# Optimization experiments

Hardware: AMD Instinct MI355X
Metric: run time of the kernel (lower is better)

Reference implementation:

```python
import jax, jax.numpy as jnp
import numpy as np

NUM_HEADS = 16
THETA = 1000.0


def apply_rope(x, positions, theta):
    """x: [B, H, S, d_k]; positions: [S] float. Interleaved-pair RoPE."""
    d = x.shape[-1]
    inv_freq = theta ** (-jnp.arange(0, d, 2, dtype=x.dtype) / d)  # [d/2]
    ang = positions[:, None] * inv_freq[None, :]                    # [S, d/2]
    cos, sin = jnp.cos(ang), jnp.sin(ang)
    x1, x2 = x[..., 0::2], x[..., 1::2]
    r1 = x1 * cos - x2 * sin
    r2 = x1 * sin + x2 * cos
    return jnp.stack([r1, r2], axis=-1).reshape(x.shape)


def setup_inputs() -> dict:
    key = jax.random.key(0)
    ks = jax.random.split(key, 5)
    B, S, D = 2, 2048, 1024
    scale = 1.0 / np.sqrt(D)
    return {
        "in_features": jax.random.normal(ks[0], (B, S, D), jnp.float32),
        "q_proj_weight": jax.random.normal(ks[1], (D, D), jnp.float32) * scale,
        "k_proj_weight": jax.random.normal(ks[2], (D, D), jnp.float32) * scale,
        "v_proj_weight": jax.random.normal(ks[3], (D, D), jnp.float32) * scale,
        "o_proj_weight": jax.random.normal(ks[4], (D, D), jnp.float32) * scale,
        "token_positions": jnp.arange(S, dtype=jnp.int32),
    }


def reference(in_features, q_proj_weight, k_proj_weight, v_proj_weight,
              o_proj_weight, token_positions):
    B, S, D = in_features.shape
    H = NUM_HEADS
    d_k = D // H

    # Original rearrange: '(d_k heads) d_model -> heads d_model d_k'
    # => first dim splits as [d_k, heads] (heads is the inner factor).
    def split_heads(w):
        return w.reshape(d_k, H, D).transpose(1, 2, 0)  # [H, D, d_k]

    Wq, Wk, Wv = split_heads(q_proj_weight), split_heads(k_proj_weight), split_heads(v_proj_weight)

    xq = jnp.einsum("bsd,hdk->bhsk", in_features, Wq)
    xk = jnp.einsum("bsd,hdk->bhsk", in_features, Wk)
    xv = jnp.einsum("bsd,hdk->bhsk", in_features, Wv)

    pos = token_positions.astype(in_features.dtype)
    xq = apply_rope(xq, pos, THETA)
    xk = apply_rope(xk, pos, THETA)

    scores = jnp.einsum("bhqk,bhmk->bhqm", xq, xk) / jnp.sqrt(
        jnp.asarray(d_k, in_features.dtype))
    causal_mask = jnp.triu(jnp.ones((S, S), bool), k=1)  # True above diagonal
    scores = jnp.where(causal_mask, -jnp.inf, scores)
    attn = jax.nn.softmax(scores, axis=-1)

    out = jnp.einsum("bhqm,bhmv->bhqv", attn, xv)        # [B, H, S, d_k]
    out = out.transpose(0, 2, 1, 3).reshape(B, S, D)     # (heads d_emb) concat
    return out @ o_proj_weight                            # [B, S, d_o]
```

## Files before the change

### kernel.cpp

```cpp
#include <hip/hip_runtime.h>

typedef unsigned short u16;
typedef unsigned int u32;
typedef __bf16 bf16x8 __attribute__((ext_vector_type(8)));
typedef float f32x4 __attribute__((ext_vector_type(4)));

#define SEQ 2048
#define DMODEL 1024
#define NH 16
#define DK 64
#define BATCH 2
#define MTOT (BATCH * SEQ)

__device__ __forceinline__ u16 f2b(float f) {
  u32 u = __float_as_uint(f);
  u += 0x7fffu + ((u >> 16) & 1u);
  return (u16)(u >> 16);
}

__device__ __forceinline__ u32 cvtpk(float lo, float hi) {
  u32 r;
  asm("v_cvt_pk_bf16_f32 %0, %1, %2" : "=v"(r) : "v"(lo), "v"(hi));
  return r;
}

__device__ __forceinline__ void gload16(const void* g, void* l) {
  __builtin_amdgcn_global_load_lds((const __attribute__((address_space(1))) u32*)g,
                                   (__attribute__((address_space(3))) u32*)l, 16, 0, 0);
}

__global__ __launch_bounds__(256) void cvt_bf16(const float* __restrict__ in,
                                                u16* __restrict__ out, int n4) {
  int i = blockIdx.x * 256 + threadIdx.x;
  if (i < n4) {
    float4 v = ((const float4*)in)[i];
    uint2 o;
    o.x = (u32)f2b(v.x) | ((u32)f2b(v.y) << 16);
    o.y = (u32)f2b(v.z) | ((u32)f2b(v.w) << 16);
    ((uint2*)out)[i] = o;
  }
}

__global__ __launch_bounds__(256) void cvt_w3(const float* __restrict__ wq,
                                              const float* __restrict__ wk,
                                              const float* __restrict__ wv,
                                              u16* __restrict__ oq,
                                              u16* __restrict__ ok,
                                              u16* __restrict__ ov) {
  const int m = blockIdx.y;
  const float* in = (m == 0) ? wq : ((m == 1) ? wk : wv);
  u16* out = (m == 0) ? oq : ((m == 1) ? ok : ov);
  const int i = blockIdx.x * 256 + threadIdx.x;
  float4 v = ((const float4*)in)[i];
  uint2 o;
  o.x = (u32)f2b(v.x) | ((u32)f2b(v.y) << 16);
  o.y = (u32)f2b(v.z) | ((u32)f2b(v.w) << 16);
  ((uint2*)out)[i] = o;
}

__global__ __launch_bounds__(256) void rope_tab_k(const int* __restrict__ tokpos,
                                                  float2* __restrict__ tab) {
  const int i = blockIdx.x * 256 + threadIdx.x;
  const int s = i >> 5, Xi = i & 31;
  const float invf = powf(1000.0f, -(float)Xi / 32.0f);
  const float ang = (float)tokpos[s] * invf;
  float sn, cs;
  sincosf(ang, &sn, &cs);
  tab[i] = make_float2(cs, sn);
}

__global__ __launch_bounds__(256) void transpose_wo(const float* __restrict__ wo,
                                                    u16* __restrict__ wot) {
  __shared__ float tile[32][33];
  const int bx = blockIdx.x * 32;
  const int by = blockIdx.y * 32;
  const int tx = threadIdx.x & 31, ty = threadIdx.x >> 5;
  for (int j = ty; j < 32; j += 8)
    tile[j][tx] = wo[(size_t)(by + j) * DMODEL + bx + tx];
  __syncthreads();
  for (int j = ty; j < 32; j += 8)
    wot[(size_t)(bx + j) * DMODEL + by + tx] = f2b(tile[tx][j]);
}

__device__ __forceinline__ void qkv_core(const u16* __restrict__ A,
                                         const u16* __restrict__ Bt,
                                         int mbase, int nbase,
                                         u16* As, u16* Bs, f32x4 acc[4][4]) {
  const int t = threadIdx.x;
  const int lane = t & 63, w = t >> 6;
  const int wr = w >> 1, wc = w & 1;
  const int l15 = lane & 15, lg = lane >> 4;
  const int srow = t >> 3;
  const int sch = (t & 7) ^ (srow & 7);
  const int rsw = l15 & 7;
  const int ASZ = 128 * 64;
  const int NIT = DMODEL / 64;

  auto stage = [&](int bufsel, int kb) {
    u16* Ad = &As[bufsel * ASZ];
    u16* Bd = &Bs[bufsel * ASZ];
#pragma unroll
    for (int j = 0; j < 4; ++j)
      gload16(&A[(size_t)(mbase + srow + 32 * j) * DMODEL + kb + sch * 8],
              &Ad[j * 2048 + t * 8]);
#pragma unroll
    for (int j = 0; j < 4; ++j)
      gload16(&Bt[(size_t)(nbase + srow + 32 * j) * DMODEL + kb + sch * 8],
              &Bd[j * 2048 + t * 8]);
  };

  auto compute = [&](int bufsel) {
    const u16* Ac = &As[bufsel * ASZ];
    const u16* Bc = &Bs[bufsel * ASZ];
#pragma unroll
    for (int kk = 0; kk < 2; ++kk) {
      bf16x8 af[4], bfr[4];
#pragma unroll
      for (int mi = 0; mi < 4; ++mi) {
        const int row = wr * 64 + mi * 16 + l15;
        af[mi] = *(const bf16x8*)&Ac[row * 64 + (((kk * 4 + lg) ^ rsw) * 8)];
      }
#pragma unroll
      for (int ni = 0; ni < 4; ++ni) {
        const int row = wc * 64 + ni * 16 + l15;
        bfr[ni] = *(const bf16x8*)&Bc[row * 64 + (((kk * 4 + lg) ^ rsw) * 8)];
      }
#pragma unroll
      for (int mi = 0; mi < 4; ++mi)
#pragma unroll
        for (int ni = 0; ni < 4; ++ni)
          acc[mi][ni] =
              __builtin_amdgcn_mfma_f32_16x16x32_bf16(af[mi], bfr[ni], acc[mi][ni], 0, 0, 0);
    }
  };

  stage(0, 0);

  for (int it = 0; it < NIT - 1; ++it) {
    const int buf = it & 1;
    stage(buf ^ 1, (it + 1) * 64);
    __builtin_amdgcn_sched_barrier(0);
    asm volatile("s_waitcnt vmcnt(8)" ::: "memory");
    __builtin_amdgcn_sched_barrier(0);
    __builtin_amdgcn_s_barrier();
    __builtin_amdgcn_sched_barrier(0);
    compute(buf);
    __builtin_amdgcn_sched_barrier(0);
    __builtin_amdgcn_s_barrier();
  }
  asm volatile("s_waitcnt vmcnt(0)" ::: "memory");
  __builtin_amdgcn_sched_barrier(0);
  __builtin_amdgcn_s_barrier();
  __builtin_amdgcn_sched_barrier(0);
  compute((DMODEL / 64 - 1) & 1);
}

__global__ __launch_bounds__(256) void gemm_qkv(
    const u16* __restrict__ Xb, const u16* __restrict__ Wqb,
    const u16* __restrict__ Wkb, const u16* __restrict__ Wvb,
    u16* __restrict__ Qb, u16* __restrict__ Kb, u16* __restrict__ Vb,
    const float2* __restrict__ tab) {
  __shared__ __align__(16) u16 As[2 * 128 * 64];
  __shared__ __align__(16) u16 Bs[2 * 128 * 64];

  const int mat = blockIdx.y >> 3;
  const int nbase = (blockIdx.y & 7) * 128;
  const int mbase = blockIdx.x * 128;
  const u16* Bt = (mat == 0) ? Wqb : ((mat == 1) ? Wkb : Wvb);

  f32x4 acc[4][4];
#pragma unroll
  for (int mi = 0; mi < 4; ++mi)
#pragma unroll
    for (int ni = 0; ni < 4; ++ni) {
      f32x4 z = {0.f, 0.f, 0.f, 0.f};
      acc[mi][ni] = z;
    }

  qkv_core(Xb, Bt, mbase, nbase, As, Bs, acc);

  const int t = threadIdx.x;
  const int lane = t & 63, w = t >> 6;
  const int wr = w >> 1, wc = w & 1;
  const int l15 = lane & 15, lg = lane >> 4;

  if (mat == 2) {
#pragma unroll
    for (int mi = 0; mi < 4; ++mi) {
#pragma unroll
      for (int r = 0; r < 4; ++r) {
        const int row = mbase + wr * 64 + mi * 16 + lg * 4 + r;
        const int bi = row >> 11, s = row & (SEQ - 1);
#pragma unroll
        for (int ni = 0; ni < 4; ++ni) {
          const int c = nbase + wc * 64 + ni * 16 + l15;
          const int hh = c & 15, vd = c >> 4;
          Vb[((size_t)((bi * NH + hh) * DK + vd)) * SEQ + s] = f2b(acc[mi][ni][r]);
        }
      }
    }
  } else {
    u16* Ob = (mat == 0) ? Qb : Kb;
    const float qscale = (mat == 0) ? 0.125f * 1.44269504088896f : 1.0f;
#pragma unroll
    for (int ni = 0; ni < 4; ni += 2) {
      const int Xi = (nbase + wc * 64 + ni * 16) >> 5;
#pragma unroll
      for (int mi = 0; mi < 4; ++mi) {
#pragma unroll
        for (int r = 0; r < 4; ++r) {
          const int row = mbase + wr * 64 + mi * 16 + lg * 4 + r;
          const int bi = row >> 11, s = row & (SEQ - 1);
          const float2 ct = tab[(s << 5) + Xi];
          const float x1 = acc[mi][ni][r], x2 = acc[mi][ni + 1][r];
          const float r1 = (x1 * ct.x - x2 * ct.y) * qscale;
          const float r2 = (x1 * ct.y + x2 * ct.x) * qscale;
          const u32 pk = (u32)f2b(r1) | ((u32)f2b(r2) << 16);
          *(u32*)&Ob[((size_t)((bi * NH + l15) * SEQ + s) << 6) + (Xi << 1)] = pk;
        }
      }
    }
  }
}

__global__ __launch_bounds__(256) void flash_attn(
    const u16* __restrict__ Qg, const u16* __restrict__ Kg,
    const u16* __restrict__ VTg, u16* __restrict__ Ag) {
  __shared__ __align__(16) u16 Ks[2][64 * 64];
  __shared__ __align__(16) u16 Vs[2][80 * 64];
  __shared__ __align__(16) u16 Ps[4][16][72];

  const int id = blockIdx.y * 32 + blockIdx.x;
  const int within = id >> 3;
  const int bh = (id & 7) * 4 + (within & 3);
  const int qt = 31 - (within >> 2);
  const int b = bh >> 4, h = bh & 15;
  const int qbase = qt * 64;

  const size_t hoff = (size_t)bh * SEQ * DK;
  const u16* Qh = Qg + hoff;
  const u16* Kh = Kg + hoff;
  const u16* VTh = VTg + hoff;

  const int t = threadIdx.x;
  const int lane = t & 63, w = t >> 6;
  const int l15 = lane & 15, lg = lane >> 4;
  const int sw = l15 & 7;

  for (int i = t; i < 2 * 16 * 64; i += 256) {
    const int bufi = i >> 10, rr = (i >> 6) & 15, cc = i & 63;
    Vs[bufi][(64 + rr) * 64 + cc] = (rr == 0) ? (u16)0x3F80 : (u16)0;
  }

  const int qrow = qbase + w * 16 + l15;
  const bf16x8 qf0 = *(const bf16x8*)&Qh[(size_t)qrow * DK + lg * 8];
  const bf16x8 qf1 = *(const bf16x8*)&Qh[(size_t)qrow * DK + 32 + lg * 8];

  f32x4 oaccT[4];
  f32x4 oacc5;
#pragma unroll
  for (int vf = 0; vf < 4; ++vf) {
    f32x4 z = {0.f, 0.f, 0.f, 0.f};
    oaccT[vf] = z;
  }
  {
    f32x4 z = {0.f, 0.f, 0.f, 0.f};
    oacc5 = z;
  }

  const int srow = t >> 3;
  const int sc = ((t & 7) ^ (srow & 7)) * 8;

  auto stageKV = [&](int bufsel, int kb) {
    gload16(&Kh[(size_t)(kb + srow) * DK + sc], &Ks[bufsel][t * 8]);
    gload16(&Kh[(size_t)(kb + srow + 32) * DK + sc], &Ks[bufsel][2048 + t * 8]);
    gload16(&VTh[(size_t)srow * SEQ + kb + sc], &Vs[bufsel][t * 8]);
    gload16(&VTh[(size_t)(srow + 32) * SEQ + kb + sc], &Vs[bufsel][2048 + t * 8]);
  };

  stageKV(0, 0);

  for (int kt = 0; kt <= qt; ++kt) {
    const int buf = kt & 1;
    if (kt < qt) {
      stageKV(buf ^ 1, (kt + 1) * 64);
      __builtin_amdgcn_sched_barrier(0);
      asm volatile("s_waitcnt vmcnt(4)" ::: "memory");
    } else {
      __builtin_amdgcn_sched_barrier(0);
      asm volatile("s_waitcnt vmcnt(0)" ::: "memory");
    }
    __builtin_amdgcn_sched_barrier(0);
    __builtin_amdgcn_s_barrier();
    __builtin_amdgcn_sched_barrier(0);

    const int kvbase = kt * 64;

    f32x4 sT[4];
    __builtin_amdgcn_s_setprio(1);
#pragma unroll
    for (int f = 0; f < 4; ++f) {
      const int row = f * 16 + l15;
      bf16x8 k0 = *(const bf16x8*)&Ks[buf][row * 64 + (lg ^ sw) * 8];
      bf16x8 k1 = *(const bf16x8*)&Ks[buf][row * 64 + ((4 + lg) ^ sw) * 8];
      f32x4 z = {0.f, 0.f, 0.f, 0.f};
      z = __builtin_amdgcn_mfma_f32_16x16x32_bf16(k0, qf0, z, 0, 0, 0);
      z = __builtin_amdgcn_mfma_f32_16x16x32_bf16(k1, qf1, z, 0, 0, 0);
      sT[f] = z;
    }
    __builtin_amdgcn_s_setprio(0);

    if (kt == qt) {
#pragma unroll
      for (int f = 0; f < 4; ++f)
#pragma unroll
        for (int r = 0; r < 4; ++r) {
          const int kvc = kvbase + f * 16 + lg * 4 + r;
          if (kvc > qrow) sT[f][r] = -1e30f;
        }
    }

#pragma unroll
    for (int f = 0; f < 4; ++f)
#pragma unroll
      for (int r = 0; r < 4; ++r) sT[f][r] = exp2f(sT[f][r]);

#pragma unroll
    for (int f = 0; f < 4; ++f) {
      uint2 pkv;
      pkv.x = cvtpk(sT[f][0], sT[f][1]);
      pkv.y = cvtpk(sT[f][2], sT[f][3]);
      *(uint2*)&Ps[w][l15][f * 16 + lg * 4] = pkv;
    }

    __builtin_amdgcn_s_setprio(1);
#pragma unroll
    for (int c = 0; c < 2; ++c) {
      const bf16x8 pb = *(const bf16x8*)&Ps[w][l15][c * 32 + lg * 8];
#pragma unroll
      for (int vf = 0; vf < 4; ++vf) {
        const bf16x8 va =
            *(const bf16x8*)&Vs[buf][(vf * 16 + l15) * 64 + ((c * 4 + lg) ^ sw) * 8];
        oaccT[vf] = __builtin_amdgcn_mfma_f32_16x16x32_bf16(va, pb, oaccT[vf], 0, 0, 0);
      }
      const bf16x8 va5 =
          *(const bf16x8*)&Vs[buf][(64 + l15) * 64 + ((c * 4 + lg) ^ sw) * 8];
      oacc5 = __builtin_amdgcn_mfma_f32_16x16x32_bf16(va5, pb, oacc5, 0, 0, 0);
    }
    __builtin_amdgcn_s_setprio(0);

    __builtin_amdgcn_sched_barrier(0);
    __builtin_amdgcn_s_barrier();
  }

  const float l = __shfl(oacc5[0], l15);
  const float inv = 1.0f / l;
  const size_t base = ((size_t)(b * SEQ + qrow)) * DMODEL + h * DK;
#pragma unroll
  for (int vf = 0; vf < 4; ++vf) {
    uint2 ov;
    ov.x = cvtpk(oaccT[vf][0] * inv, oaccT[vf][1] * inv);
    ov.y = cvtpk(oaccT[vf][2] * inv, oaccT[vf][3] * inv);
    *(uint2*)&Ag[base + vf * 16 + lg * 4] = ov;
  }
}

__global__ __launch_bounds__(256) void gemm_out(const u16* __restrict__ Ab,
                                                const u16* __restrict__ Wotb,
                                                float* __restrict__ Co) {
  __shared__ __align__(16) u16 As[64 * 64];
  __shared__ __align__(16) u16 Bs[128 * 64];
  const int mbase = blockIdx.x * 64, nbase = blockIdx.y * 128;

  const int t = threadIdx.x;
  const int lane = t & 63, w = t >> 6;
  const int wr = w >> 1, wc = w & 1;
  const int l15 = lane & 15, lg = lane >> 4;
  const int srow = t >> 3;
  const int sch = (t & 7) ^ (srow & 7);
  const int rsw = l15 & 7;

  f32x4 acc[2][4];
#pragma unroll
  for (int mi = 0; mi < 2; ++mi)
#pragma unroll
    for (int ni = 0; ni < 4; ++ni) {
      f32x4 z = {0.f, 0.f, 0.f, 0.f};
      acc[mi][ni] = z;
    }

  for (int kb = 0; kb < DMODEL; kb += 64) {
    gload16(&Ab[(size_t)(mbase + srow) * DMODEL + kb + sch * 8], &As[t * 8]);
    gload16(&Ab[(size_t)(mbase + 32 + srow) * DMODEL + kb + sch * 8], &As[2048 + t * 8]);
#pragma unroll
    for (int j = 0; j < 4; ++j)
      gload16(&Wotb[(size_t)(nbase + srow + 32 * j) * DMODEL + kb + sch * 8],
              &Bs[j * 2048 + t * 8]);
    __syncthreads();
#pragma unroll
    for (int kk = 0; kk < 2; ++kk) {
      bf16x8 af[2], bfr[4];
#pragma unroll
      for (int mi = 0; mi < 2; ++mi) {
        const int row = wr * 32 + mi * 16 + l15;
        af[mi] = *(const bf16x8*)&As[row * 64 + (((kk * 4 + lg) ^ rsw) * 8)];
      }
#pragma unroll
      for (int ni = 0; ni < 4; ++ni) {
        const int row = wc * 64 + ni * 16 + l15;
        bfr[ni] = *(const bf16x8*)&Bs[row * 64 + (((kk * 4 + lg) ^ rsw) * 8)];
      }
#pragma unroll
      for (int mi = 0; mi < 2; ++mi)
#pragma unroll
        for (int ni = 0; ni < 4; ++ni)
          acc[mi][ni] =
              __builtin_amdgcn_mfma_f32_16x16x32_bf16(af[mi], bfr[ni], acc[mi][ni], 0, 0, 0);
    }
    __syncthreads();
  }

#pragma unroll
  for (int mi = 0; mi < 2; ++mi) {
#pragma unroll
    for (int r = 0; r < 4; ++r) {
      const int row = mbase + wr * 32 + mi * 16 + lg * 4 + r;
#pragma unroll
      for (int ni = 0; ni < 4; ++ni) {
        const int c = nbase + wc * 64 + ni * 16 + l15;
        Co[(size_t)row * DMODEL + c] = acc[mi][ni][r];
      }
    }
  }
}

extern "C" void kernel_launch(void* const* d_in, const int* in_sizes, int n_in,
                              void* d_out, int out_size, void* d_ws, size_t ws_size,
                              hipStream_t stream) {
  const float* X = (const float*)d_in[0];
  const float* Wq = (const float*)d_in[1];
  const float* Wk = (const float*)d_in[2];
  const float* Wv = (const float*)d_in[3];
  const float* Wo = (const float*)d_in[4];
  const int* tokpos = (const int*)d_in[5];
  float* out = (float*)d_out;

  u16* p = (u16*)d_ws;
  u16* Xb = p;   p += (size_t)MTOT * DMODEL;
  u16* Wqb = p;  p += (size_t)DMODEL * DMODEL;
  u16* Wkb = p;  p += (size_t)DMODEL * DMODEL;
  u16* Wvb = p;  p += (size_t)DMODEL * DMODEL;
  u16* Wotb = p; p += (size_t)DMODEL * DMODEL;
  u16* Qb = p;   p += (size_t)BATCH * NH * SEQ * DK;
  u16* Kb = p;   p += (size_t)BATCH * NH * SEQ * DK;
  u16* Vb = p;   p += (size_t)BATCH * NH * SEQ * DK;
  float2* tab = (float2*)(p + 512);
  u16* Ab = Xb;

  cvt_bf16<<<4096, 256, 0, stream>>>(X, Xb, (MTOT * DMODEL) / 4);
  cvt_w3<<<dim3(1024, 3), 256, 0, stream>>>(Wq, Wk, Wv, Wqb, Wkb, Wvb);
  transpose_wo<<<dim3(32, 32), 256, 0, stream>>>(Wo, Wotb);
  rope_tab_k<<<(SEQ * 32) / 256, 256, 0, stream>>>(tokpos, tab);

  gemm_qkv<<<dim3(32, 24), 256, 0, stream>>>(Xb, Wqb, Wkb, Wvb, Qb, Kb, Vb, tab);
  flash_attn<<<dim3(32, 32), 256, 0, stream>>>(Qb, Kb, Vb, Ab);
  gemm_out<<<dim3(64, 8), 256, 0, stream>>>(Ab, Wotb, out);
}
```

Before: 131.3 us.

## Merge prep kernels and single-buffer flash attention KV for higher occupancy

Combines the input/weight bf16 conversion and RoPE table kernels into a single launch to cut launch overhead. In flash attention, removes the double-buffered K/V staging in favor of a single LDS buffer loaded synchronously each iteration, and sets launch bounds to allow 5 blocks per CU. This trades exposed global-load latency for higher occupancy and less LDS per block.

```diff
diff --git a/kernel.cpp b/kernel.cpp
--- a/kernel.cpp
+++ b/kernel.cpp
@@ -29,44 +29,40 @@
                                    (__attribute__((address_space(3))) u32*)l, 16, 0, 0);
 }
 
-__global__ __launch_bounds__(256) void cvt_bf16(const float* __restrict__ in,
-                                                u16* __restrict__ out, int n4) {
-  int i = blockIdx.x * 256 + threadIdx.x;
-  if (i < n4) {
+__global__ __launch_bounds__(256) void cvt_all(
+    const float* __restrict__ X, const float* __restrict__ wq,
+    const float* __restrict__ wk, const float* __restrict__ wv,
+    const int* __restrict__ tokpos, u16* __restrict__ Xb,
+    u16* __restrict__ oq, u16* __restrict__ ok, u16* __restrict__ ov,
+    float2* __restrict__ tab) {
+  const int bid = blockIdx.x;
+  if (bid < 7168) {
+    const float* in;
+    u16* out;
+    int i;
+    if (bid < 4096) {
+      in = X; out = Xb; i = bid * 256 + threadIdx.x;
+    } else {
+      const int j = bid - 4096;
+      const int m = j >> 10;
+      in = (m == 0) ? wq : ((m == 1) ? wk : wv);
+      out = (m == 0) ? oq : ((m == 1) ? ok : ov);
+      i = (j & 1023) * 256 + threadIdx.x;
+    }
     float4 v = ((const float4*)in)[i];
     uint2 o;
     o.x = (u32)f2b(v.x) | ((u32)f2b(v.y) << 16);
     o.y = (u32)f2b(v.z) | ((u32)f2b(v.w) << 16);
     ((uint2*)out)[i] = o;
-  }
-}
-
-__global__ __launch_bounds__(256) void cvt_w3(const float* __restrict__ wq,
-                                              const float* __restrict__ wk,
-                                              const float* __restrict__ wv,
-                                              u16* __restrict__ oq,
-                                              u16* __restrict__ ok,
-                                              u16* __restrict__ ov) {
-  const int m = blockIdx.y;
-  const float* in = (m == 0) ? wq : ((m == 1) ? wk : wv);
-  u16* out = (m == 0) ? oq : ((m == 1) ? ok : ov);
-  const int i = blockIdx.x * 256 + threadIdx.x;
-  float4 v = ((const float4*)in)[i];
-  uint2 o;
-  o.x = (u32)f2b(v.x) | ((u32)f2b(v.y) << 16);
-  o.y = (u32)f2b(v.z) | ((u32)f2b(v.w) << 16);
-  ((uint2*)out)[i] = o;
-}
-
-__global__ __launch_bounds__(256) void rope_tab_k(const int* __restrict__ tokpos,
-                                                  float2* __restrict__ tab) {
-  const int i = blockIdx.x * 256 + threadIdx.x;
-  const int s = i >> 5, Xi = i & 31;
-  const float invf = powf(1000.0f, -(float)Xi / 32.0f);
-  const float ang = (float)tokpos[s] * invf;
-  float sn, cs;
-  sincosf(ang, &sn, &cs);
-  tab[i] = make_float2(cs, sn);
+  } else {
+    const int i = (bid - 7168) * 256 + threadIdx.x;
+    const int s = i >> 5, Xi = i & 31;
+    const float invf = powf(1000.0f, -(float)Xi / 32.0f);
+    const float ang = (float)tokpos[s] * invf;
+    float sn, cs;
+    sincosf(ang, &sn, &cs);
+    tab[i] = make_float2(cs, sn);
+  }
 }
 
 __global__ __launch_bounds__(256) void transpose_wo(const float* __restrict__ wo,
@@ -223,11 +219,11 @@
   }
 }
 
-__global__ __launch_bounds__(256) void flash_attn(
+__global__ __launch_bounds__(256, 5) void flash_attn(
     const u16* __restrict__ Qg, const u16* __restrict__ Kg,
     const u16* __restrict__ VTg, u16* __restrict__ Ag) {
-  __shared__ __align__(16) u16 Ks[2][64 * 64];
-  __shared__ __align__(16) u16 Vs[2][80 * 64];
+  __shared__ __align__(16) u16 Ks[64 * 64];
+  __shared__ __align__(16) u16 Vs[80 * 64];
   __shared__ __align__(16) u16 Ps[4][16][72];
 
   const int id = blockIdx.y * 32 + blockIdx.x;
@@ -247,9 +243,9 @@
   const int l15 = lane & 15, lg = lane >> 4;
   const int sw = l15 & 7;
 
-  for (int i = t; i < 2 * 16 * 64; i += 256) {
-    const int bufi = i >> 10, rr = (i >> 6) & 15, cc = i & 63;
-    Vs[bufi][(64 + rr) * 64 + cc] = (rr == 0) ? (u16)0x3F80 : (u16)0;
+  for (int i = t; i < 16 * 64; i += 256) {
+    const int rr = i >> 6, cc = i & 63;
+    Vs[(64 + rr) * 64 + cc] = (rr == 0) ? (u16)0x3F80 : (u16)0;
   }
 
   const int qrow = qbase + w * 16 + l15;
@@ -271,38 +267,23 @@
   const int srow = t >> 3;
   const int sc = ((t & 7) ^ (srow & 7)) * 8;
 
-  auto stageKV = [&](int bufsel, int kb) {
-    gload16(&Kh[(size_t)(kb + srow) * DK + sc], &Ks[bufsel][t * 8]);
-    gload16(&Kh[(size_t)(kb + srow + 32) * DK + sc], &Ks[bufsel][2048 + t * 8]);
-    gload16(&VTh[(size_t)srow * SEQ + kb + sc], &Vs[bufsel][t * 8]);
-    gload16(&VTh[(size_t)(srow + 32) * SEQ + kb + sc], &Vs[bufsel][2048 + t * 8]);
-  };
-
-  stageKV(0, 0);
-
   for (int kt = 0; kt <= qt; ++kt) {
-    const int buf = kt & 1;
-    if (kt < qt) {
-      stageKV(buf ^ 1, (kt + 1) * 64);
-      __builtin_amdgcn_sched_barrier(0);
-      asm volatile("s_waitcnt vmcnt(4)" ::: "memory");
-    } else {
-      __builtin_amdgcn_sched_barrier(0);
-      asm volatile("s_waitcnt vmcnt(0)" ::: "memory");
-    }
-    __builtin_amdgcn_sched_barrier(0);
+    const int kvbase = kt * 64;
+    __syncthreads();
+    gload16(&Kh[(size_t)(kvbase + srow) * DK + sc], &Ks[t * 8]);
+    gload16(&Kh[(size_t)(kvbase + srow + 32) * DK + sc], &Ks[2048 + t * 8]);
+    gload16(&VTh[(size_t)srow * SEQ + kvbase + sc], &Vs[t * 8]);
+    gload16(&VTh[(size_t)(srow + 32) * SEQ + kvbase + sc], &Vs[2048 + t * 8]);
+    asm volatile("s_waitcnt vmcnt(0)" ::: "memory");
     __builtin_amdgcn_s_barrier();
-    __builtin_amdgcn_sched_barrier(0);
-
-    const int kvbase = kt * 64;
 
     f32x4 sT[4];
     __builtin_amdgcn_s_setprio(1);
 #pragma unroll
     for (int f = 0; f < 4; ++f) {
       const int row = f * 16 + l15;
-      bf16x8 k0 = *(const bf16x8*)&Ks[buf][row * 64 + (lg ^ sw) * 8];
-      bf16x8 k1 = *(const bf16x8*)&Ks[buf][row * 64 + ((4 + lg) ^ sw) * 8];
+      bf16x8 k0 = *(const bf16x8*)&Ks[row * 64 + (lg ^ sw) * 8];
+      bf16x8 k1 = *(const bf16x8*)&Ks[row * 64 + ((4 + lg) ^ sw) * 8];
       f32x4 z = {0.f, 0.f, 0.f, 0.f};
       z = __builtin_amdgcn_mfma_f32_16x16x32_bf16(k0, qf0, z, 0, 0, 0);
       z = __builtin_amdgcn_mfma_f32_16x16x32_bf16(k1, qf1, z, 0, 0, 0);
@@ -340,17 +321,14 @@
 #pragma unroll
       for (int vf = 0; vf < 4; ++vf) {
         const bf16x8 va =
-            *(const bf16x8*)&Vs[buf][(vf * 16 + l15) * 64 + ((c * 4 + lg) ^ sw) * 8];
+            *(const bf16x8*)&Vs[(vf * 16 + l15) * 64 + ((c * 4 + lg) ^ sw) * 8];
         oaccT[vf] = __builtin_amdgcn_mfma_f32_16x16x32_bf16(va, pb, oaccT[vf], 0, 0, 0);
       }
       const bf16x8 va5 =
-          *(const bf16x8*)&Vs[buf][(64 + l15) * 64 + ((c * 4 + lg) ^ sw) * 8];
+          *(const bf16x8*)&Vs[(64 + l15) * 64 + ((c * 4 + lg) ^ sw) * 8];
       oacc5 = __builtin_amdgcn_mfma_f32_16x16x32_bf16(va5, pb, oacc5, 0, 0, 0);
     }
     __builtin_amdgcn_s_setprio(0);
-
-    __builtin_amdgcn_sched_barrier(0);
-    __builtin_amdgcn_s_barrier();
   }
 
   const float l = __shfl(oacc5[0], l15);
@@ -457,10 +435,8 @@
   float2* tab = (float2*)(p + 512);
   u16* Ab = Xb;
 
-  cvt_bf16<<<4096, 256, 0, stream>>>(X, Xb, (MTOT * DMODEL) / 4);
-  cvt_w3<<<dim3(1024, 3), 256, 0, stream>>>(Wq, Wk, Wv, Wqb, Wkb, Wvb);
+  cvt_all<<<7424, 256, 0, stream>>>(X, Wq, Wk, Wv, tokpos, Xb, Wqb, Wkb, Wvb, tab);
   transpose_wo<<<dim3(32, 32), 256, 0, stream>>>(Wo, Wotb);
-  rope_tab_k<<<(SEQ * 32) / 256, 256, 0, stream>>>(tokpos, tab);
 
   gemm_qkv<<<dim3(32, 24), 256, 0, stream>>>(Xb, Wqb, Wkb, Wvb, Qb, Kb, Vb, tab);
   flash_attn<<<dim3(32, 32), 256, 0, stream>>>(Qb, Kb, Vb, Ab);
```

After: 127.4 us. -3.0%, faster.
